# Performance work log

Hardware: AMD Instinct MI355X
Metric: run time of the kernel (lower is better)

## Reference

```python
import jax, jax.numpy as jnp
import numpy as np

SCALE = 4
PAD = 128


def setup_inputs() -> dict:
    key = jax.random.key(0)
    x = jax.random.normal(key, (32, 512, 512), dtype=jnp.float32)
    return {"x": x}


def reference(x) -> jnp.ndarray:
    # Pad both spatial dims by PAD with zeros, then nearest-neighbor upsample
    # by SCALE in both dims. Equivalent to the per-sample pad+tile+transpose
    # chain, but done as two batched repeats over the whole batch.
    sx = jnp.pad(x, ((0, 0), (PAD, PAD), (PAD, PAD)))  # [B, H+2p, W+2p]
    sx = jnp.repeat(sx, SCALE, axis=1)                  # rows repeated
    sx = jnp.repeat(sx, SCALE, axis=2)                  # cols repeated
    return sx
```

## Files before the change

kernel.cpp:

```cpp
#include <hip/hip_runtime.h>


typedef float vfloat4 __attribute__((ext_vector_type(4)));

constexpr int OUTW   = 3072;
constexpr int IN     = 512;
constexpr int Q_LO   = 128;
constexpr int Q_HI   = 640;
constexpr int ROW_LO = 512;
constexpr int ROW_HI = 2560;

__global__ __launch_bounds__(256) void scale_layer_kernel(
    const float* __restrict__ x, float* __restrict__ out) {
    const int i = blockIdx.x;
    const int b = blockIdx.y;

    vfloat4* __restrict__ orow = reinterpret_cast<vfloat4*>(
        out + ((size_t)b * OUTW + i) * OUTW);

    const bool in_row = (i >= ROW_LO) && (i < ROW_HI);
    const float* irow = x + ((size_t)b * IN + ((i - ROW_LO) >> 2)) * IN;

    #pragma unroll
    for (int k = 0; k < 3; ++k) {
        const int jq = (int)threadIdx.x + k * 256;
        float v = 0.0f;
        if (in_row && jq >= Q_LO && jq < Q_HI) {
            v = irow[jq - Q_LO];
        }
        vfloat4 vv = {v, v, v, v};
        orow[jq] = vv;
    }
}

extern "C" void kernel_launch(void* const* d_in, const int* in_sizes, int n_in,
                              void* d_out, int out_size, void* d_ws, size_t ws_size,
                              hipStream_t stream) {
    const float* x = (const float*)d_in[0];
    float* out = (float*)d_out;
    dim3 grid(OUTW, 32);
    scale_layer_kernel<<<grid, 256, 0, stream>>>(x, out);
}
```

Baseline: 1.196 ms.

## Split output into zero-fill regions and interior copy with grid-stride blocks

Replaces the one-block-per-output-row launch with a 3D grid. Three z-slices zero-fill the top, bottom and side padding regions with grid-stride loops, and the fourth slice reads each input row once and writes it to the four replicated output rows. This removes per-element boundary branching and input loads from the padding regions and cuts the block count. In exchange the z-slices do uneven amounts of work, and the side-padding writes are short 2KB strided segments.

```diff
diff --git a/kernel.cpp b/kernel.cpp
--- a/kernel.cpp
+++ b/kernel.cpp
@@ -3,33 +3,55 @@
 
 typedef float vfloat4 __attribute__((ext_vector_type(4)));
 
-constexpr int OUTW   = 3072;
-constexpr int IN     = 512;
-constexpr int Q_LO   = 128;
-constexpr int Q_HI   = 640;
-constexpr int ROW_LO = 512;
-constexpr int ROW_HI = 2560;
+constexpr int OUTW = 3072;
+constexpr int QW   = OUTW / 4;
+constexpr int IN   = 512;
+constexpr int GX   = 64;
+constexpr int NTHR = 256;
 
-__global__ __launch_bounds__(256) void scale_layer_kernel(
+constexpr int TOPQ  = 512 * QW;
+constexpr int SIDEQ = 2048 * 256;
+
+__global__ __launch_bounds__(NTHR) void scale_layer_kernel(
     const float* __restrict__ x, float* __restrict__ out) {
-    const int i = blockIdx.x;
     const int b = blockIdx.y;
+    const int z = blockIdx.z;
+    const int t = (int)(blockIdx.x * NTHR + threadIdx.x);
+    const int stride = GX * NTHR;
 
-    vfloat4* __restrict__ orow = reinterpret_cast<vfloat4*>(
-        out + ((size_t)b * OUTW + i) * OUTW);
+    float* __restrict__ obase = out + (size_t)b * OUTW * OUTW;
+    vfloat4* __restrict__ oq = reinterpret_cast<vfloat4*>(obase);
+    const vfloat4 zero = {0.f, 0.f, 0.f, 0.f};
 
-    const bool in_row = (i >= ROW_LO) && (i < ROW_HI);
-    const float* irow = x + ((size_t)b * IN + ((i - ROW_LO) >> 2)) * IN;
-
-    #pragma unroll
-    for (int k = 0; k < 3; ++k) {
-        const int jq = (int)threadIdx.x + k * 256;
-        float v = 0.0f;
-        if (in_row && jq >= Q_LO && jq < Q_HI) {
-            v = irow[jq - Q_LO];
+    if (z == 0) {
+        for (int idx = t; idx < TOPQ; idx += stride) oq[idx] = zero;
+    } else if (z == 1) {
+        vfloat4* p = oq + (size_t)2560 * QW;
+        for (int idx = t; idx < TOPQ; idx += stride) p[idx] = zero;
+    } else if (z == 2) {
+        for (int idx = t; idx < SIDEQ; idx += stride) {
+            const int row = idx >> 8;
+            const int q   = idx & 255;
+            const int jq  = q + (q >= 128 ? 512 : 0);
+            oq[(size_t)(512 + row) * QW + jq] = zero;
         }
-        vfloat4 vv = {v, v, v, v};
-        orow[jq] = vv;
+    } else {
+        const int r0 = (int)blockIdx.x * 8;
+        const int tt = (int)threadIdx.x;
+        const float* __restrict__ img = x + (size_t)b * IN * IN;
+        for (int r = r0; r < r0 + 8; ++r) {
+            const float v0 = img[(size_t)r * IN + tt];
+            const float v1 = img[(size_t)r * IN + tt + 256];
+            const vfloat4 a = {v0, v0, v0, v0};
+            const vfloat4 c = {v1, v1, v1, v1};
+            const int i0 = 512 + r * 4;
+            #pragma unroll
+            for (int rr = 0; rr < 4; ++rr) {
+                vfloat4* orow = oq + (size_t)(i0 + rr) * QW;
+                orow[128 + tt] = a;
+                orow[384 + tt] = c;
+            }
+        }
     }
 }
 
@@ -38,6 +60,6 @@
                               hipStream_t stream) {
     const float* x = (const float*)d_in[0];
     float* out = (float*)d_out;
-    dim3 grid(OUTW, 32);
-    scale_layer_kernel<<<grid, 256, 0, stream>>>(x, out);
+    dim3 grid(GX, 32, 4);
+    scale_layer_kernel<<<grid, NTHR, 0, stream>>>(x, out);
 }
```

After: 1.193 ms. No clear change (-0.2%).
